# Performance work log

Measured on AMD Instinct MI355X. Metric: run time of the kernel, lower is better.

## Reference

```python
import jax, jax.numpy as jnp
import numpy as np

N, E = 50000, 800000          # nodes, edges
DIN, HEAD, HD = 128, 4, 16    # input dim, heads, per-head dim
DOUT = HEAD * HD              # 64 = head*hd
NEG_SLOPE = 0.01              # torch LeakyReLU default


def _lin(key, fan_in, fan_out):
    # torch nn.Linear default init: U(-1/sqrt(fan_in), 1/sqrt(fan_in))
    kw, kb = jax.random.split(key)
    s = 1.0 / np.sqrt(fan_in)
    W = jax.random.uniform(kw, (fan_in, fan_out), jnp.float32, -s, s)
    b = jax.random.uniform(kb, (fan_out,), jnp.float32, -s, s)
    return W, b


def setup_inputs() -> dict:
    key = jax.random.key(0)
    ks = jax.random.split(key, 8)
    x = jax.random.normal(ks[0], (N, DIN), jnp.float32)
    src = jax.random.randint(ks[1], (E,), 0, N, jnp.int32)
    dst = jax.random.randint(ks[2], (E,), 0, N, jnp.int32)
    Ws, bs = _lin(ks[3], DIN, DOUT)   # relation_aware src linear
    Wd, bd = _lin(ks[4], DIN, DOUT)   # relation_aware dst linear
    Wl, bl = _lin(ks[5], DIN, DOUT)   # w_liner
    Wa, ba = _lin(ks[6], 3 * HD, 1)   # atten
    return dict(x=x, src=src, dst=dst, Ws=Ws, bs=bs, Wd=Wd, bd=bd,
                Wl=Wl, bl=bl, Wa=Wa, ba=ba)


def reference(x, src, dst, Ws, bs, Wd, bd, Wl, bl, Wa, ba):
    # sign_edges: relation-aware per-edge feature edge_sum  [E, DOUT]
    er = jnp.tanh(x[src] @ Ws + bs + (x[dst] @ Wd + bd))

    # w_liner on node features  [N, DOUT]
    h = x @ Wl + bl

    # message: per-edge, per-head concat + linear + leakyrelu score
    sf = h[src].reshape(E, HEAD, HD)
    df = h[dst].reshape(E, HEAD, HD)
    ef = er.reshape(E, HEAD, HD)
    z = jnp.concatenate([sf, df, ef], axis=-1)        # [E, HEAD, 3*HD]
    a = z @ Wa + ba                                    # [E, HEAD, 1]
    a = jnp.where(a >= 0, a, NEG_SLOPE * a)            # leaky relu

    # reduce: mailbox softmax over incoming edges of each dst node
    m = jax.ops.segment_max(a, dst, num_segments=N)    # [N, HEAD, 1]
    m = jnp.where(jnp.isfinite(m), m, 0.0)             # empty mailboxes -> 0
    e = jnp.exp(a - m[dst])
    s = jax.ops.segment_sum(e, dst, num_segments=N)    # [N, HEAD, 1]
    attn = e / jnp.maximum(s[dst], 1e-38)

    out = jax.ops.segment_sum(attn * sf, dst, num_segments=N)
    out = out.reshape(N, DOUT)                         # [N, head*hd]

    # edge_s: mean of edge_sum over incoming edges per node
    deg = jax.ops.segment_sum(jnp.ones((E, 1), x.dtype), dst, num_segments=N)
    edge_s = jax.ops.segment_sum(er, dst, num_segments=N) / jnp.maximum(deg, 1.0)

    return (edge_s, out, h)  # if_sum=False branch: h already [N, head*hd]
```

## Files before the change

### kernel.cpp

```cpp
#include <hip/hip_runtime.h>
#include <math.h>

#define DIN   128
#define DOUT  64
#define NHEAD 4
#define HD    16
#define BKT_SH 7
#define BKT_SZ 128

typedef __attribute__((ext_vector_type(8))) short bf16x8;
typedef __attribute__((ext_vector_type(8))) unsigned short u16x8;
typedef __attribute__((ext_vector_type(4))) float f32x4;

__device__ __forceinline__ unsigned short f2bf(float f) {
    union { float f; unsigned u; } v; v.f = f;
    unsigned r = v.u + 0x7FFF + ((v.u >> 16) & 1);
    return (unsigned short)(r >> 16);
}
__device__ __forceinline__ float bf2f(unsigned short s) {
    union { unsigned u; float f; } v; v.u = ((unsigned)s) << 16; return v.f;
}

__global__ __launch_bounds__(256)
void k_init(const float* __restrict__ Ws, const float* __restrict__ Wd,
            const float* __restrict__ Wl, short* __restrict__ wT,
            int* __restrict__ bucket_cnt, int NBK) {
    const int bid = blockIdx.x, tid = threadIdx.x;
    if (bid < 96) {
        const int idx = bid * 256 + tid;
        const int n = idx >> 7, k = idx & 127;
        float v;
        if (n < 64)       v = Ws[k * DOUT + n];
        else if (n < 128) v = Wd[k * DOUT + (n - 64)];
        else              v = Wl[k * DOUT + (n - 128)];
        wT[idx] = (short)f2bf(v);
        return;
    }
    const int i = (bid - 96) * 256 + tid;
    if (i <= NBK) bucket_cnt[i] = 0;
}

__global__ __launch_bounds__(256)
void k_proj_cnt(const float* __restrict__ x, const short* __restrict__ wT,
                const float* __restrict__ bs, const float* __restrict__ bd,
                const float* __restrict__ bl, const float* __restrict__ Wa,
                unsigned short* __restrict__ packed_bf,
                float* __restrict__ xd, float* __restrict__ alpha_s,
                float* __restrict__ alpha_d, float* __restrict__ h_out, int N,
                const int* __restrict__ dst, int* __restrict__ bucket_cnt,
                int E, int NPJ, int NCB, int NBK) {
    __shared__ short xs[64 * 136];
    __shared__ short wtl[48 * 512];
    __shared__ int  lhist[392];
    const int bid = blockIdx.x, tid = threadIdx.x;

    if (bid & 1) {
        const int ci = bid >> 1;
        if (ci >= NCB) return;
        for (int i = tid; i < NBK; i += 256) lhist[i] = 0;
        __syncthreads();
        const int base0 = ci * 4096;
#pragma unroll
        for (int k = 0; k < 4; ++k) {
            const int e0 = base0 + k * 1024 + tid * 4;
            if (e0 + 3 < E) {
                const int4 d = *(const int4*)&dst[e0];
                atomicAdd(&lhist[d.x >> BKT_SH], 1);
                atomicAdd(&lhist[d.y >> BKT_SH], 1);
                atomicAdd(&lhist[d.z >> BKT_SH], 1);
                atomicAdd(&lhist[d.w >> BKT_SH], 1);
            } else {
                for (int e = e0; e < E; ++e) atomicAdd(&lhist[dst[e] >> BKT_SH], 1);
            }
        }
        __syncthreads();
        for (int i = tid; i < NBK; i += 256)
            if (lhist[i]) atomicAdd(&bucket_cnt[i], lhist[i]);
        return;
    }

    const int pj = bid >> 1;
    if (pj >= NPJ) return;
    const int wave = tid >> 6, lane = tid & 63;
    const int lam = lane & 15, g = lane >> 4;
    const int n0 = pj * 64;

    {
        const int r = tid >> 2, c0 = (tid & 3) * 32;
        const int nn = n0 + r;
#pragma unroll
        for (int j = 0; j < 8; ++j) {
            float4 v = make_float4(0.f, 0.f, 0.f, 0.f);
            if (nn < N) v = ((const float4*)x)[(size_t)nn * 32 + (c0 >> 2) + j];
            short4 h4;
            h4.x = (short)f2bf(v.x); h4.y = (short)f2bf(v.y);
            h4.z = (short)f2bf(v.z); h4.w = (short)f2bf(v.w);
            *(short4*)&xs[r * 136 + c0 + j * 4] = h4;
        }
    }
#pragma unroll
    for (int k = 0; k < 12; ++k) {
        const int s = k * 256 + tid;
        const int f = s >> 6, l = s & 63;
        const int c = f >> 2, ks = f & 3;
        const int go = (c * 16 + (l & 15)) * 128 + ks * 32 + (l >> 4) * 8;
        *(u16x8*)&wtl[s * 8] = *(const u16x8*)&wT[go];
    }
    __syncthreads();

    bf16x8 afr[4];
#pragma unroll
    for (int ks = 0; ks < 4; ++ks)
        afr[ks] = *(const bf16x8*)&xs[(wave * 16 + lam) * 136 + ks * 32 + g * 8];

    f32x4 acc[12];
#pragma unroll
    for (int c = 0; c < 12; ++c) acc[c] = (f32x4){0.f, 0.f, 0.f, 0.f};

#pragma unroll
    for (int c = 0; c < 12; ++c) {
#pragma unroll
        for (int ks = 0; ks < 4; ++ks) {
            const bf16x8 b = *(const bf16x8*)&wtl[(((c * 4 + ks) << 6) + lane) * 8];
            acc[c] = __builtin_amdgcn_mfma_f32_16x16x32_bf16(afr[ks], b, acc[c], 0, 0, 0);
        }
    }

    float bsv[4], bdv[4], blv[4];
#pragma unroll
    for (int c = 0; c < 4; ++c) {
        bsv[c] = bs[c * 16 + lam];
        bdv[c] = bd[c * 16 + lam];
        blv[c] = bl[c * 16 + lam];
    }
    const float waS = Wa[lam], waD = Wa[16 + lam];
    const int cc_base = (lam >> 2), t_sl = lam & 3;

#pragma unroll
    for (int i = 0; i < 4; ++i) {
        const int node = n0 + wave * 16 + g * 4 + i;
        float xsv[4], xdv[4], hv[4];
#pragma unroll
        for (int c = 0; c < 4; ++c) {
            xsv[c] = acc[c][i]     + bsv[c];
            xdv[c] = acc[4 + c][i] + bdv[c];
            hv[c]  = acc[8 + c][i] + blv[c];
        }
        float p0 = hv[0] * waS, p1 = hv[1] * waS, p2 = hv[2] * waS, p3 = hv[3] * waS;
        float q0 = hv[0] * waD, q1 = hv[1] * waD, q2 = hv[2] * waD, q3 = hv[3] * waD;
#pragma unroll
        for (int off = 1; off < 16; off <<= 1) {
            p0 += __shfl_xor(p0, off); p1 += __shfl_xor(p1, off);
            p2 += __shfl_xor(p2, off); p3 += __shfl_xor(p3, off);
            q0 += __shfl_xor(q0, off); q1 += __shfl_xor(q1, off);
            q2 += __shfl_xor(q2, off); q3 += __shfl_xor(q3, off);
        }
        if (node < N) {
            const size_t rowb = (size_t)node * 128;
#pragma unroll
            for (int c = 0; c < 4; ++c) {
                const int cc = c * 4 + cc_base;
                packed_bf[rowb + cc * 8 + t_sl]     = f2bf(xsv[c]);
                packed_bf[rowb + cc * 8 + 4 + t_sl] = f2bf(hv[c]);
                xd   [(size_t)node * DOUT + c * 16 + lam] = xdv[c];
                h_out[(size_t)node * DOUT + c * 16 + lam] = hv[c];
            }
            if (lam == 0) {
                *(f32x4*)&alpha_s[(size_t)node * NHEAD] = (f32x4){p0, p1, p2, p3};
                *(f32x4*)&alpha_d[(size_t)node * NHEAD] = (f32x4){q0, q1, q2, q3};
            }
        }
    }
}

__global__ __launch_bounds__(512)
void k_scan_buckets(const int* __restrict__ bucket_cnt,
                    int* __restrict__ bucket_base, int* __restrict__ bucket_cursor,
                    int NBK) {
    __shared__ int wsum[8];
    const int tid = threadIdx.x, lane = tid & 63, wid = tid >> 6;
    int v = (tid < NBK) ? bucket_cnt[tid] : 0;
    int incl = v;
#pragma unroll
    for (int off = 1; off < 64; off <<= 1) {
        int t = __shfl_up(incl, off);
        if (lane >= off) incl += t;
    }
    if (lane == 63) wsum[wid] = incl;
    __syncthreads();
    if (tid < 8) {
        int t = wsum[tid];
#pragma unroll
        for (int off = 1; off < 8; off <<= 1) {
            int u = __shfl_up(t, off);
            if (tid >= off) t += u;
        }
        wsum[tid] = t;
    }
    __syncthreads();
    const int base = (wid > 0) ? wsum[wid - 1] : 0;
    const int excl = incl - v + base;
    if (tid < NBK) {
        bucket_base[tid]   = excl;
        bucket_cursor[tid] = excl;
    }
    if (tid == 0) bucket_base[NBK] = wsum[7];
}

__global__ __launch_bounds__(256)
void k_bucket_scatter(const int* __restrict__ src, const int* __restrict__ dst,
                      int* __restrict__ bucket_cursor, int2* __restrict__ pairs,
                      int E, int NBK) {
    __shared__ int lhist[392];
    __shared__ int lcur[392];
    const int tid = threadIdx.x;
    const int base0 = blockIdx.x * 4096;
    for (int i = tid; i < NBK; i += 256) lhist[i] = 0;
    __syncthreads();
#pragma unroll
    for (int k = 0; k < 4; ++k) {
        const int e0 = base0 + k * 1024 + tid * 4;
        if (e0 + 3 < E) {
            const int4 d = *(const int4*)&dst[e0];
            atomicAdd(&lhist[d.x >> BKT_SH], 1);
            atomicAdd(&lhist[d.y >> BKT_SH], 1);
            atomicAdd(&lhist[d.z >> BKT_SH], 1);
            atomicAdd(&lhist[d.w >> BKT_SH], 1);
        } else {
            for (int e = e0; e < E; ++e) atomicAdd(&lhist[dst[e] >> BKT_SH], 1);
        }
    }
    __syncthreads();
    for (int i = tid; i < NBK; i += 256)
        lcur[i] = lhist[i] ? atomicAdd(&bucket_cursor[i], lhist[i]) : 0;
    __syncthreads();
#pragma unroll
    for (int k = 0; k < 4; ++k) {
        const int e0 = base0 + k * 1024 + tid * 4;
        if (e0 + 3 < E) {
            const int4 s = *(const int4*)&src[e0];
            const int4 d = *(const int4*)&dst[e0];
            int p;
            p = atomicAdd(&lcur[d.x >> BKT_SH], 1); pairs[p] = make_int2(s.x, d.x);
            p = atomicAdd(&lcur[d.y >> BKT_SH], 1); pairs[p] = make_int2(s.y, d.y);
            p = atomicAdd(&lcur[d.z >> BKT_SH], 1); pairs[p] = make_int2(s.z, d.z);
            p = atomicAdd(&lcur[d.w >> BKT_SH], 1); pairs[p] = make_int2(s.w, d.w);
        } else {
            for (int e = e0; e < E; ++e) {
                const int d = dst[e];
                const int p = atomicAdd(&lcur[d >> BKT_SH], 1);
                pairs[p] = make_int2(src[e], d);
            }
        }
    }
}

__global__ __launch_bounds__(256)
void k_bucket_rank(const int2* __restrict__ pairs, const int* __restrict__ bucket_base,
                   int* __restrict__ row_ptr, int* __restrict__ srcs,
                   int N, int NBK) {
    __shared__ int hist[BKT_SZ];
    __shared__ int cursor[BKT_SZ];
    __shared__ int wtot[2];
    const int b = blockIdx.x, tid = threadIdx.x;
    const int n0 = b << BKT_SH;
    const int ebase = bucket_base[b];
    const int ecnt  = bucket_base[b + 1] - ebase;

    if (tid < BKT_SZ) hist[tid] = 0;
    __syncthreads();
    for (int i = tid; i < ecnt; i += 256)
        atomicAdd(&hist[pairs[ebase + i].y & (BKT_SZ - 1)], 1);
    __syncthreads();

    int v = 0, incl = 0;
    const int lane = tid & 63, wid = tid >> 6;
    if (tid < BKT_SZ) {
        v = hist[tid];
        incl = v;
#pragma unroll
        for (int off = 1; off < 64; off <<= 1) {
            int t = __shfl_up(incl, off);
            if (lane >= off) incl += t;
        }
        if (lane == 63) wtot[wid] = incl;
    }
    __syncthreads();
    if (tid < BKT_SZ) {
        const int excl = incl - v + ((wid == 1) ? wtot[0] : 0);
        if (n0 + tid < N) row_ptr[n0 + tid] = ebase + excl;
        cursor[tid] = excl;
    }
    if (b == NBK - 1 && tid == 0) row_ptr[N] = bucket_base[NBK];
    __syncthreads();

    for (int i = tid; i < ecnt; i += 256) {
        const int2 pr = pairs[ebase + i];
        const int slot = atomicAdd(&cursor[pr.y & (BKT_SZ - 1)], 1);
        srcs[ebase + slot] = pr.x;
    }
}

__global__ __launch_bounds__(256, 8)
void k_aggregate(const int* __restrict__ row_ptr, const int* __restrict__ srcs,
                 const unsigned short* __restrict__ packed_bf,
                 const float* __restrict__ xd,
                 const float* __restrict__ alpha_s, const float* __restrict__ alpha_d,
                 const float* __restrict__ Wa, const float* __restrict__ ba,
                 float* __restrict__ edge_s, float* __restrict__ out, int N) {
    const int lane = threadIdx.x & 63;
    const int n = blockIdx.x * 4 + (threadIdx.x >> 6);
    if (n >= N) return;
    const int g = lane >> 4, lam = lane & 15;
    const int hd = lam >> 2, q = lam & 3;

    const int start = row_ptr[n];
    const int end   = row_ptr[n + 1];
    const int deg = end - start;
    const int last = end - 1;

    const float4 xd4 = *(const float4*)&xd[(size_t)n * DOUT + lam * 4];
    const float4 wa4 = *(const float4*)&Wa[32 + q * 4];
    const float adb  = alpha_d[n * NHEAD + hd] + ba[0];

    float es0=0.f,es1=0.f,es2=0.f,es3=0.f;
    float o0=0.f,o1=0.f,o2=0.f,o3=0.f;
    float s = 0.f;

    const int niter = (deg + 3) >> 2;
    int e = start + g;

    float vm0=0.f, vm1=0.f, vm2=0.f;
    u16x8 pk0=(u16x8){0,0,0,0,0,0,0,0}, pk1=pk0, pk2=pk0;
    float as0=0.f, as1=0.f, as2=0.f;
    if (niter > 0) {
        {
            vm0 = (e < end) ? 1.f : 0.f;
            const int sn = srcs[min(e, last)];
            pk0 = *(const u16x8*)&packed_bf[(size_t)sn * 128 + lam * 8];
            as0 = alpha_s[sn * NHEAD + hd];
        }
        {
            const int e1 = e + 4;
            vm1 = (e1 < end) ? 1.f : 0.f;
            const int sn = srcs[min(e1, last)];
            pk1 = *(const u16x8*)&packed_bf[(size_t)sn * 128 + lam * 8];
            as1 = alpha_s[sn * NHEAD + hd];
        }
        {
            const int e2 = e + 8;
            vm2 = (e2 < end) ? 1.f : 0.f;
            const int sn = srcs[min(e2, last)];
            pk2 = *(const u16x8*)&packed_bf[(size_t)sn * 128 + lam * 8];
            as2 = alpha_s[sn * NHEAD + hd];
        }
    }

    for (int it = 0; it < niter; ++it) {
        float vmn = 0.f, asn = 0.f;
        u16x8 pkn = (u16x8){0,0,0,0,0,0,0,0};
        const int e3 = e + 12;
        if (it + 3 < niter) {
            vmn = (e3 < end) ? 1.f : 0.f;
            const int sn = srcs[min(e3, last)];
            pkn = *(const u16x8*)&packed_bf[(size_t)sn * 128 + lam * 8];
            asn = alpha_s[sn * NHEAD + hd];
        }

        const float t0 = __expf(2.f * (bf2f(pk0[0]) + xd4.x));
        const float t1 = __expf(2.f * (bf2f(pk0[1]) + xd4.y));
        const float t2 = __expf(2.f * (bf2f(pk0[2]) + xd4.z));
        const float t3 = __expf(2.f * (bf2f(pk0[3]) + xd4.w));
        const float er0 = fmaf(-2.f, __builtin_amdgcn_rcpf(t0 + 1.f), 1.f);
        const float er1 = fmaf(-2.f, __builtin_amdgcn_rcpf(t1 + 1.f), 1.f);
        const float er2 = fmaf(-2.f, __builtin_amdgcn_rcpf(t2 + 1.f), 1.f);
        const float er3 = fmaf(-2.f, __builtin_amdgcn_rcpf(t3 + 1.f), 1.f);
        es0 = fmaf(er0, vm0, es0); es1 = fmaf(er1, vm0, es1);
        es2 = fmaf(er2, vm0, es2); es3 = fmaf(er3, vm0, es3);

        float p = er0 * wa4.x;
        p = fmaf(er1, wa4.y, p);
        p = fmaf(er2, wa4.z, p);
        p = fmaf(er3, wa4.w, p);
        p += __shfl_xor(p, 1);
        p += __shfl_xor(p, 2);

        float a = as0 + adb + p;
        a = (a >= 0.f) ? a : 0.01f * a;
        const float w = __expf(a) * vm0;
        s += w;
        o0 = fmaf(w, bf2f(pk0[4]), o0); o1 = fmaf(w, bf2f(pk0[5]), o1);
        o2 = fmaf(w, bf2f(pk0[6]), o2); o3 = fmaf(w, bf2f(pk0[7]), o3);

        vm0 = vm1; pk0 = pk1; as0 = as1;
        vm1 = vm2; pk1 = pk2; as1 = as2;
        vm2 = vmn; pk2 = pkn; as2 = asn;
        e += 4;
    }

#pragma unroll
    for (int off = 16; off < 64; off <<= 1) {
        es0 += __shfl_xor(es0, off); es1 += __shfl_xor(es1, off);
        es2 += __shfl_xor(es2, off); es3 += __shfl_xor(es3, off);
        o0  += __shfl_xor(o0,  off); o1  += __shfl_xor(o1,  off);
        o2  += __shfl_xor(o2,  off); o3  += __shfl_xor(o3,  off);
        s   += __shfl_xor(s,   off);
    }

    if (g == 0) {
        const float inv_s = __builtin_amdgcn_rcpf(fmaxf(s, 1e-38f));
        const float inv_d = __builtin_amdgcn_rcpf(fmaxf((float)deg, 1.0f));
        const size_t od = (size_t)n * DOUT + lam * 4;
        *(f32x4*)&out[od]    = (f32x4){o0 * inv_s, o1 * inv_s, o2 * inv_s, o3 * inv_s};
        *(f32x4*)&edge_s[od] = (f32x4){es0 * inv_d, es1 * inv_d, es2 * inv_d, es3 * inv_d};
    }
}

extern "C" void kernel_launch(void* const* d_in, const int* in_sizes, int n_in,
                              void* d_out, int out_size, void* d_ws, size_t ws_size,
                              hipStream_t stream) {
    const float* x  = (const float*)d_in[0];
    const int*   src= (const int*)  d_in[1];
    const int*   dst= (const int*)  d_in[2];
    const float* Ws = (const float*)d_in[3];
    const float* bs = (const float*)d_in[4];
    const float* Wd = (const float*)d_in[5];
    const float* bd = (const float*)d_in[6];
    const float* Wl = (const float*)d_in[7];
    const float* bl = (const float*)d_in[8];
    const float* Wa = (const float*)d_in[9];
    const float* ba = (const float*)d_in[10];

    const int N = in_sizes[0] / DIN;
    const int E = in_sizes[1];
    const int NBK = (N + BKT_SZ - 1) >> BKT_SH;

    float* out_f = (float*)d_out;
    float* edge_s_out = out_f;
    float* out_attn   = out_f + (size_t)N * DOUT;
    float* h_out      = out_f + 2 * (size_t)N * DOUT;

    char* ws = (char*)d_ws;
    size_t o = 0;
    unsigned short* packed_bf = (unsigned short*)(ws + o); o += (size_t)N * 128 * 2;
    float* xd      = (float*)(ws + o); o += (size_t)N * DOUT * 4;
    float* alpha_s = (float*)(ws + o); o += (size_t)N * NHEAD * 4;
    float* alpha_d = (float*)(ws + o); o += (size_t)N * NHEAD * 4;
    int*   row_ptr = (int*)  (ws + o); o += (size_t)(N + 1) * 4;
    int*   srcs    = (int*)  (ws + o); o += (size_t)E * 4;
    int2*  pairs   = (int2*) (ws + o); o += (size_t)E * 8;
    int*   bucket_cnt    = (int*)(ws + o); o += 512 * 4;
    int*   bucket_base   = (int*)(ws + o); o += 513 * 4;
    int*   bucket_cursor = (int*)(ws + o); o += 512 * 4;
    short* wT      = (short*)(ws + o); o += (size_t)192 * 128 * 2;

    k_init<<<96 + (NBK + 256) / 256, 256, 0, stream>>>(Ws, Wd, Wl, wT, bucket_cnt, NBK);

    const int NPJ = (N + 63) / 64;
    const int NCB = (E + 4095) / 4096;
    const int GC  = 2 * ((NPJ > NCB) ? NPJ : NCB);
    k_proj_cnt<<<GC, 256, 0, stream>>>(x, wT, bs, bd, bl, Wa,
                                       packed_bf, xd, alpha_s, alpha_d, h_out, N,
                                       dst, bucket_cnt, E, NPJ, NCB, NBK);

    k_scan_buckets<<<1, 512, 0, stream>>>(bucket_cnt, bucket_base, bucket_cursor, NBK);

    k_bucket_scatter<<<NCB, 256, 0, stream>>>(src, dst, bucket_cursor, pairs, E, NBK);

    k_bucket_rank<<<NBK, 256, 0, stream>>>(pairs, bucket_base, row_ptr, srcs, N, NBK);

    k_aggregate<<<(N + 3) / 4, 256, 0, stream>>>(row_ptr, srcs, packed_bf, xd,
                                                 alpha_s, alpha_d, Wa, ba,
                                                 edge_s_out, out_attn, N);
}
```

Before: 110.8 us.

## Move bucket count before projection and overlap edge scatter with node projection

The dst histogram now runs in the weight-transpose kernel, after a memset of the counters, and the bucket scan runs right after it. The edge scatter into buckets then shares a launch with the node projection GEMM in interleaved blocks. This removes one kernel launch and lets the scatter overlap with projection compute instead of running alone afterwards. Separately, the tanh exponent in the aggregate loop is rewritten to use exp2 with a prescaled log2(e) factor folded into an FMA. The cost is an extra memset call and more shared memory in the fused projection/scatter kernel.

```diff
diff --git a/kernel.cpp b/kernel.cpp
--- a/kernel.cpp
+++ b/kernel.cpp
@@ -22,9 +22,11 @@
 }
 
 __global__ __launch_bounds__(256)
-void k_init(const float* __restrict__ Ws, const float* __restrict__ Wd,
-            const float* __restrict__ Wl, short* __restrict__ wT,
-            int* __restrict__ bucket_cnt, int NBK) {
+void k_cnt_wt(const float* __restrict__ Ws, const float* __restrict__ Wd,
+              const float* __restrict__ Wl, short* __restrict__ wT,
+              const int* __restrict__ dst, int* __restrict__ bucket_cnt,
+              int E, int NBK) {
+    __shared__ int lhist[392];
     const int bid = blockIdx.x, tid = threadIdx.x;
     if (bid < 96) {
         const int idx = bid * 256 + tid;
@@ -36,30 +38,84 @@
         wT[idx] = (short)f2bf(v);
         return;
     }
-    const int i = (bid - 96) * 256 + tid;
-    if (i <= NBK) bucket_cnt[i] = 0;
+    const int ci = bid - 96;
+    for (int i = tid; i < NBK; i += 256) lhist[i] = 0;
+    __syncthreads();
+    const int base0 = ci * 4096;
+#pragma unroll
+    for (int k = 0; k < 4; ++k) {
+        const int e0 = base0 + k * 1024 + tid * 4;
+        if (e0 + 3 < E) {
+            const int4 d = *(const int4*)&dst[e0];
+            atomicAdd(&lhist[d.x >> BKT_SH], 1);
+            atomicAdd(&lhist[d.y >> BKT_SH], 1);
+            atomicAdd(&lhist[d.z >> BKT_SH], 1);
+            atomicAdd(&lhist[d.w >> BKT_SH], 1);
+        } else {
+            for (int e = e0; e < E; ++e) atomicAdd(&lhist[dst[e] >> BKT_SH], 1);
+        }
+    }
+    __syncthreads();
+    for (int i = tid; i < NBK; i += 256)
+        if (lhist[i]) atomicAdd(&bucket_cnt[i], lhist[i]);
+}
+
+__global__ __launch_bounds__(512)
+void k_scan_buckets(const int* __restrict__ bucket_cnt,
+                    int* __restrict__ bucket_base, int* __restrict__ bucket_cursor,
+                    int NBK) {
+    __shared__ int wsum[8];
+    const int tid = threadIdx.x, lane = tid & 63, wid = tid >> 6;
+    int v = (tid < NBK) ? bucket_cnt[tid] : 0;
+    int incl = v;
+#pragma unroll
+    for (int off = 1; off < 64; off <<= 1) {
+        int t = __shfl_up(incl, off);
+        if (lane >= off) incl += t;
+    }
+    if (lane == 63) wsum[wid] = incl;
+    __syncthreads();
+    if (tid < 8) {
+        int t = wsum[tid];
+#pragma unroll
+        for (int off = 1; off < 8; off <<= 1) {
+            int u = __shfl_up(t, off);
+            if (tid >= off) t += u;
+        }
+        wsum[tid] = t;
+    }
+    __syncthreads();
+    const int base = (wid > 0) ? wsum[wid - 1] : 0;
+    const int excl = incl - v + base;
+    if (tid < NBK) {
+        bucket_base[tid]   = excl;
+        bucket_cursor[tid] = excl;
+    }
+    if (tid == 0) bucket_base[NBK] = wsum[7];
 }
 
 __global__ __launch_bounds__(256)
-void k_proj_cnt(const float* __restrict__ x, const short* __restrict__ wT,
-                const float* __restrict__ bs, const float* __restrict__ bd,
-                const float* __restrict__ bl, const float* __restrict__ Wa,
-                unsigned short* __restrict__ packed_bf,
-                float* __restrict__ xd, float* __restrict__ alpha_s,
-                float* __restrict__ alpha_d, float* __restrict__ h_out, int N,
-                const int* __restrict__ dst, int* __restrict__ bucket_cnt,
-                int E, int NPJ, int NCB, int NBK) {
+void k_proj_scatter(const float* __restrict__ x, const short* __restrict__ wT,
+                    const float* __restrict__ bs, const float* __restrict__ bd,
+                    const float* __restrict__ bl, const float* __restrict__ Wa,
+                    unsigned short* __restrict__ packed_bf,
+                    float* __restrict__ xd, float* __restrict__ alpha_s,
+                    float* __restrict__ alpha_d, float* __restrict__ h_out, int N,
+                    const int* __restrict__ src, const int* __restrict__ dst,
+                    int* __restrict__ bucket_cursor, int2* __restrict__ pairs,
+                    int E, int NPJ, int NSC, int NBK) {
     __shared__ short xs[64 * 136];
     __shared__ short wtl[48 * 512];
-    __shared__ int  lhist[392];
+    __shared__ int lhist[392];
+    __shared__ int lcur[392];
     const int bid = blockIdx.x, tid = threadIdx.x;
 
     if (bid & 1) {
         const int ci = bid >> 1;
-        if (ci >= NCB) return;
+        if (ci >= NSC) return;
+        const int base0 = ci * 4096;
         for (int i = tid; i < NBK; i += 256) lhist[i] = 0;
         __syncthreads();
-        const int base0 = ci * 4096;
 #pragma unroll
         for (int k = 0; k < 4; ++k) {
             const int e0 = base0 + k * 1024 + tid * 4;
@@ -75,7 +131,27 @@
         }
         __syncthreads();
         for (int i = tid; i < NBK; i += 256)
-            if (lhist[i]) atomicAdd(&bucket_cnt[i], lhist[i]);
+            lcur[i] = lhist[i] ? atomicAdd(&bucket_cursor[i], lhist[i]) : 0;
+        __syncthreads();
+#pragma unroll
+        for (int k = 0; k < 4; ++k) {
+            const int e0 = base0 + k * 1024 + tid * 4;
+            if (e0 + 3 < E) {
+                const int4 s = *(const int4*)&src[e0];
+                const int4 d = *(const int4*)&dst[e0];
+                int p;
+                p = atomicAdd(&lcur[d.x >> BKT_SH], 1); pairs[p] = make_int2(s.x, d.x);
+                p = atomicAdd(&lcur[d.y >> BKT_SH], 1); pairs[p] = make_int2(s.y, d.y);
+                p = atomicAdd(&lcur[d.z >> BKT_SH], 1); pairs[p] = make_int2(s.z, d.z);
+                p = atomicAdd(&lcur[d.w >> BKT_SH], 1); pairs[p] = make_int2(s.w, d.w);
+            } else {
+                for (int e = e0; e < E; ++e) {
+                    const int d = dst[e];
+                    const int p = atomicAdd(&lcur[d >> BKT_SH], 1);
+                    pairs[p] = make_int2(src[e], d);
+                }
+            }
+        }
         return;
     }
 
@@ -168,88 +244,6 @@
             if (lam == 0) {
                 *(f32x4*)&alpha_s[(size_t)node * NHEAD] = (f32x4){p0, p1, p2, p3};
                 *(f32x4*)&alpha_d[(size_t)node * NHEAD] = (f32x4){q0, q1, q2, q3};
-            }
-        }
-    }
-}
-
-__global__ __launch_bounds__(512)
-void k_scan_buckets(const int* __restrict__ bucket_cnt,
-                    int* __restrict__ bucket_base, int* __restrict__ bucket_cursor,
-                    int NBK) {
-    __shared__ int wsum[8];
-    const int tid = threadIdx.x, lane = tid & 63, wid = tid >> 6;
-    int v = (tid < NBK) ? bucket_cnt[tid] : 0;
-    int incl = v;
-#pragma unroll
-    for (int off = 1; off < 64; off <<= 1) {
-        int t = __shfl_up(incl, off);
-        if (lane >= off) incl += t;
-    }
-    if (lane == 63) wsum[wid] = incl;
-    __syncthreads();
-    if (tid < 8) {
-        int t = wsum[tid];
-#pragma unroll
-        for (int off = 1; off < 8; off <<= 1) {
-            int u = __shfl_up(t, off);
-            if (tid >= off) t += u;
-        }
-        wsum[tid] = t;
-    }
-    __syncthreads();
-    const int base = (wid > 0) ? wsum[wid - 1] : 0;
-    const int excl = incl - v + base;
-    if (tid < NBK) {
-        bucket_base[tid]   = excl;
-        bucket_cursor[tid] = excl;
-    }
-    if (tid == 0) bucket_base[NBK] = wsum[7];
-}
-
-__global__ __launch_bounds__(256)
-void k_bucket_scatter(const int* __restrict__ src, const int* __restrict__ dst,
-                      int* __restrict__ bucket_cursor, int2* __restrict__ pairs,
-                      int E, int NBK) {
-    __shared__ int lhist[392];
-    __shared__ int lcur[392];
-    const int tid = threadIdx.x;
-    const int base0 = blockIdx.x * 4096;
-    for (int i = tid; i < NBK; i += 256) lhist[i] = 0;
-    __syncthreads();
-#pragma unroll
-    for (int k = 0; k < 4; ++k) {
-        const int e0 = base0 + k * 1024 + tid * 4;
-        if (e0 + 3 < E) {
-            const int4 d = *(const int4*)&dst[e0];
-            atomicAdd(&lhist[d.x >> BKT_SH], 1);
-            atomicAdd(&lhist[d.y >> BKT_SH], 1);
-            atomicAdd(&lhist[d.z >> BKT_SH], 1);
-            atomicAdd(&lhist[d.w >> BKT_SH], 1);
-        } else {
-            for (int e = e0; e < E; ++e) atomicAdd(&lhist[dst[e] >> BKT_SH], 1);
-        }
-    }
-    __syncthreads();
-    for (int i = tid; i < NBK; i += 256)
-        lcur[i] = lhist[i] ? atomicAdd(&bucket_cursor[i], lhist[i]) : 0;
-    __syncthreads();
-#pragma unroll
-    for (int k = 0; k < 4; ++k) {
-        const int e0 = base0 + k * 1024 + tid * 4;
-        if (e0 + 3 < E) {
-            const int4 s = *(const int4*)&src[e0];
-            const int4 d = *(const int4*)&dst[e0];
-            int p;
-            p = atomicAdd(&lcur[d.x >> BKT_SH], 1); pairs[p] = make_int2(s.x, d.x);
-            p = atomicAdd(&lcur[d.y >> BKT_SH], 1); pairs[p] = make_int2(s.y, d.y);
-            p = atomicAdd(&lcur[d.z >> BKT_SH], 1); pairs[p] = make_int2(s.z, d.z);
-            p = atomicAdd(&lcur[d.w >> BKT_SH], 1); pairs[p] = make_int2(s.w, d.w);
-        } else {
-            for (int e = e0; e < E; ++e) {
-                const int d = dst[e];
-                const int p = atomicAdd(&lcur[d >> BKT_SH], 1);
-                pairs[p] = make_int2(src[e], d);
             }
         }
     }
@@ -319,7 +313,10 @@
     const int deg = end - start;
     const int last = end - 1;
 
+    const float L2E2 = 2.8853900817779268f;
     const float4 xd4 = *(const float4*)&xd[(size_t)n * DOUT + lam * 4];
+    const float4 xdp = make_float4(xd4.x * L2E2, xd4.y * L2E2,
+                                   xd4.z * L2E2, xd4.w * L2E2);
     const float4 wa4 = *(const float4*)&Wa[32 + q * 4];
     const float adb  = alpha_d[n * NHEAD + hd] + ba[0];
 
@@ -367,10 +364,10 @@
             asn = alpha_s[sn * NHEAD + hd];
         }
 
-        const float t0 = __expf(2.f * (bf2f(pk0[0]) + xd4.x));
-        const float t1 = __expf(2.f * (bf2f(pk0[1]) + xd4.y));
-        const float t2 = __expf(2.f * (bf2f(pk0[2]) + xd4.z));
-        const float t3 = __expf(2.f * (bf2f(pk0[3]) + xd4.w));
+        const float t0 = exp2f(fmaf(bf2f(pk0[0]), L2E2, xdp.x));
+        const float t1 = exp2f(fmaf(bf2f(pk0[1]), L2E2, xdp.y));
+        const float t2 = exp2f(fmaf(bf2f(pk0[2]), L2E2, xdp.z));
+        const float t3 = exp2f(fmaf(bf2f(pk0[3]), L2E2, xdp.w));
         const float er0 = fmaf(-2.f, __builtin_amdgcn_rcpf(t0 + 1.f), 1.f);
         const float er1 = fmaf(-2.f, __builtin_amdgcn_rcpf(t1 + 1.f), 1.f);
         const float er2 = fmaf(-2.f, __builtin_amdgcn_rcpf(t2 + 1.f), 1.f);
@@ -454,18 +451,19 @@
     int*   bucket_cursor = (int*)(ws + o); o += 512 * 4;
     short* wT      = (short*)(ws + o); o += (size_t)192 * 128 * 2;
 
-    k_init<<<96 + (NBK + 256) / 256, 256, 0, stream>>>(Ws, Wd, Wl, wT, bucket_cnt, NBK);
+    hipMemsetAsync(bucket_cnt, 0, 512 * 4, stream);
+
+    const int NCB = (E + 4095) / 4096;
+    k_cnt_wt<<<96 + NCB, 256, 0, stream>>>(Ws, Wd, Wl, wT, dst, bucket_cnt, E, NBK);
+
+    k_scan_buckets<<<1, 512, 0, stream>>>(bucket_cnt, bucket_base, bucket_cursor, NBK);
 
     const int NPJ = (N + 63) / 64;
-    const int NCB = (E + 4095) / 4096;
     const int GC  = 2 * ((NPJ > NCB) ? NPJ : NCB);
-    k_proj_cnt<<<GC, 256, 0, stream>>>(x, wT, bs, bd, bl, Wa,
-                                       packed_bf, xd, alpha_s, alpha_d, h_out, N,
-                                       dst, bucket_cnt, E, NPJ, NCB, NBK);
-
-    k_scan_buckets<<<1, 512, 0, stream>>>(bucket_cnt, bucket_base, bucket_cursor, NBK);
-
-    k_bucket_scatter<<<NCB, 256, 0, stream>>>(src, dst, bucket_cursor, pairs, E, NBK);
+    k_proj_scatter<<<GC, 256, 0, stream>>>(x, wT, bs, bd, bl, Wa,
+                                           packed_bf, xd, alpha_s, alpha_d, h_out, N,
+                                           src, dst, bucket_cursor, pairs,
+                                           E, NPJ, NCB, NBK);
 
     k_bucket_rank<<<NBK, 256, 0, stream>>>(pairs, bucket_base, row_ptr, srcs, N, NBK);
 
```

New measurement: 111.3 us. About the same (+0.5%).
